# Kernel optimization log

Hardware: AMD Instinct MI355X
Metric: run time of the kernel (lower is better)

The kernel has to match this reference:

```python
import jax, jax.numpy as jnp
import numpy as np

BS, HID, INP, SPAN, OUT, DAYS = 32768, 128, 64, 8, 2, 20


def _init(key, shape, fan_in):
    # mimic torch default uniform(-1/sqrt(fan), 1/sqrt(fan)) init
    bound = 1.0 / np.sqrt(fan_in)
    return jax.random.uniform(key, shape, jnp.float32, -bound, bound)


def setup_inputs() -> dict:
    key = jax.random.key(0)
    ks = jax.random.split(key, 11)
    return {
        "hx": jax.random.normal(ks[0], (BS, HID), jnp.float32),
        # GRUCell params (PyTorch layout: gates stacked [r, z, n])
        "w_ih": _init(ks[1], (3 * HID, INP), HID),
        "w_hh": _init(ks[2], (3 * HID, HID), HID),
        "b_ih": _init(ks[3], (3 * HID,), HID),
        "b_hh": _init(ks[4], (3 * HID,), HID),
        # fc_in: hid -> input
        "fc_in_w": _init(ks[5], (INP, HID), HID),
        "fc_in_b": _init(ks[6], (INP,), HID),
        # fc_out: hid -> out
        "fc_out_w": _init(ks[7], (OUT, HID), HID),
        "fc_out_b": _init(ks[8], (OUT,), HID),
        # num_span_layer: hid -> num_span_classes
        "span_w": _init(ks[9], (SPAN, HID), HID),
        "span_b": _init(ks[10], (SPAN,), HID),
    }


def _gru_cell(x, h, w_ih, w_hh, b_ih, b_hh):
    gi = x @ w_ih.T + b_ih  # [B, 3H]
    gh = h @ w_hh.T + b_hh  # [B, 3H]
    i_r, i_z, i_n = jnp.split(gi, 3, axis=-1)
    h_r, h_z, h_n = jnp.split(gh, 3, axis=-1)
    r = jax.nn.sigmoid(i_r + h_r)
    z = jax.nn.sigmoid(i_z + h_z)
    n = jnp.tanh(i_n + r * h_n)
    return (1.0 - z) * n + z * h


def reference(hx, w_ih, w_hh, b_ih, b_hh, fc_in_w, fc_in_b,
              fc_out_w, fc_out_b, span_w, span_b):
    num_spans = jax.nn.softmax(hx @ span_w.T + span_b, axis=-1)  # [B, SPAN]
    x0 = jnp.zeros((hx.shape[0], fc_in_w.shape[0]), hx.dtype)  # zero first input

    def step(carry, _):
        h, x = carry
        h = _gru_cell(x, h, w_ih, w_hh, b_ih, b_hh)
        x = jax.nn.relu(h @ fc_in_w.T + fc_in_b)
        out = jax.nn.softmax(h @ fc_out_w.T + fc_out_b, axis=-1)  # [B, OUT]
        return (h, x), out

    _, outs = jax.lax.scan(step, (hx, x0), None, length=DAYS)  # [DAYS, B, OUT]
    outputs = jnp.transpose(outs, (1, 0, 2))  # [B, DAYS, OUT]
    return num_spans, outputs
```

## Files before the change

### kernel.cpp

```cpp
#include <hip/hip_runtime.h>
#include <hip/hip_bf16.h>

#define HID 128
#define INP 64
#define SPANN 8
#define NOUT 2
#define DAYS 20
#define RT 4
#define ROWS (16*RT)
#define NTH 512

typedef __attribute__((ext_vector_type(8))) short short8;
typedef __attribute__((ext_vector_type(4))) float f32x4;
typedef __attribute__((ext_vector_type(2))) float f32x2;
typedef unsigned int u32;
typedef __attribute__((ext_vector_type(2))) u32 u32x2;
typedef unsigned short u16;

#define MFMA(a,b,c) __builtin_amdgcn_mfma_f32_16x16x32_bf16(a,b,c,0,0,0)
#define RCPF(x)  __builtin_amdgcn_rcpf(x)
#define EXP2F(x) __builtin_amdgcn_exp2f(x)
#define LOG2E  1.4426950408889634f
#define LOG2E2 2.8853900817779268f

__device__ __forceinline__ u32 pack2(float a, float b){
    __hip_bfloat162 h = __float22bfloat162_rn(float2{a, b});
    u32 r; __builtin_memcpy(&r, &h, 4); return r;
}
__device__ __forceinline__ float sigf(float x){ return RCPF(1.0f + EXP2F(-LOG2E * x)); }
__device__ __forceinline__ float tanhf_(float x){ return fmaf(-2.0f, RCPF(1.0f + EXP2F(LOG2E2 * x)), 1.0f); }

union frag_u { short8 s; u32 w[4]; };
__device__ __forceinline__ short8 ldfrag(const float* p){
    const f32x4 a = *(const f32x4*)p;
    const f32x4 b = *(const f32x4*)(p+4);
    frag_u f;
    f.w[0] = pack2(a[0],a[1]); f.w[1] = pack2(a[2],a[3]);
    f.w[2] = pack2(b[0],b[1]); f.w[3] = pack2(b[2],b[3]);
    return f.s;
}


__global__ __launch_bounds__(NTH, 2) void gru_mfma(
    const float* __restrict__ hx, const float* __restrict__ w_ih,
    const float* __restrict__ w_hh, const float* __restrict__ b_ih,
    const float* __restrict__ b_hh, const float* __restrict__ fc_in_w,
    const float* __restrict__ fc_in_b, const float* __restrict__ fc_out_w,
    const float* __restrict__ fc_out_b, const float* __restrict__ span_w,
    const float* __restrict__ span_b, float* __restrict__ out, int bs)
{
    __shared__ u16 hL[2][RT*2048];
    __shared__ u16 xL[RT*1024];
    __shared__ u16 finL[4*4*64*8];
    __shared__ __attribute__((aligned(16))) float diffP[ROWS][8];

    const int tid = threadIdx.x;
    const int wid = tid >> 6;
    const int l   = tid & 63;
    const int r15 = l & 15;
    const int hi  = l >> 4;
    const int row0 = blockIdx.x * ROWS;
    const int mB  = wid & 3;
    const int rtB_off = wid >> 2;

    short8 whhR[4], whhZ[4], whhN[4];
    short8 wihR[2], wihZ[2], wihN[2];
    const int g0 = wid*16 + r15;
    #pragma unroll
    for (int ks = 0; ks < 4; ++ks){
        whhR[ks] = ldfrag(w_hh + (size_t)(      g0)*HID + ks*32 + hi*8);
        whhZ[ks] = ldfrag(w_hh + (size_t)(128 + g0)*HID + ks*32 + hi*8);
        whhN[ks] = ldfrag(w_hh + (size_t)(256 + g0)*HID + ks*32 + hi*8);
    }
    #pragma unroll
    for (int ks = 0; ks < 2; ++ks){
        wihR[ks] = ldfrag(w_ih + (size_t)(      g0)*INP + ks*32 + hi*8);
        wihZ[ks] = ldfrag(w_ih + (size_t)(128 + g0)*INP + ks*32 + hi*8);
        wihN[ks] = ldfrag(w_ih + (size_t)(256 + g0)*INP + ks*32 + hi*8);
    }

    for (int s = tid; s < 1024; s += NTH) {
        const int mt = s >> 8, ks = (s >> 6) & 3, ll = s & 63;
        short8 f = ldfrag(fc_in_w + (size_t)(mt*16 + (ll&15))*HID + ks*32 + (ll>>4)*8);
        *((short8*)finL + s) = f;
    }

    f32x4 bRv, bZv, bNiv, bNhv, fbv, wd4;
    const int c0 = wid*16 + hi*4;
    #pragma unroll
    for (int q = 0; q < 4; ++q){
        const int g = c0 + q;
        bRv[q]  = b_ih[g]       + b_hh[g];
        bZv[q]  = b_ih[128 + g] + b_hh[128 + g];
        bNiv[q] = b_ih[256 + g];
        bNhv[q] = b_hh[256 + g];
        fbv[q]  = fc_in_b[mB*16 + hi*4 + q];
        wd4[q]  = fc_out_w[g] - fc_out_w[HID + g];
    }
    const float bd = fc_out_b[0] - fc_out_b[1];

    const int wu32  = (wid>>1)*256 + (((wid&1)*2 + (hi>>1))*16 + r15)*4 + (hi&1)*2;
    const int xwu32 = (mB >>1)*256 + (((mB &1)*2 + (hi>>1))*16 + r15)*4 + (hi&1)*2;

    f32x4 hOld0, hOld1, hOld2, hOld3;
    {
        #define LOADH(RTG, HO) do { \
            const f32x4 h4 = *(const f32x4*)(hx + (size_t)(row0 + (RTG)*16 + r15)*HID + c0); \
            HO = h4; \
            u32x2 wv; wv[0] = pack2(h4[0], h4[1]); wv[1] = pack2(h4[2], h4[3]); \
            *(u32x2*)((u32*)&hL[0][(RTG)*2048] + wu32) = wv; } while(0)
        LOADH(0, hOld0); LOADH(1, hOld1); LOADH(2, hOld2); LOADH(3, hOld3);
        #undef LOADH
        u32* xb = (u32*)&xL[0];
        for (int i = tid; i < RT*512; i += NTH) xb[i] = 0u;
    }
    __syncthreads();

    if (wid < 4){
        const short8 zz = {0,0,0,0,0,0,0,0};
        short8 spw[4];
        #pragma unroll
        for (int ks = 0; ks < 4; ++ks)
            spw[ks] = (r15 < SPANN) ? ldfrag(span_w + (size_t)r15*HID + ks*32 + hi*8) : zz;
        f32x4 acc = {0.f,0.f,0.f,0.f};
        #pragma unroll
        for (int q = 0; q < 4; ++q) if (hi < 2) acc[q] = span_b[hi*4 + q];
        const short8* hf = (const short8*)&hL[0][wid*2048];
        #pragma unroll
        for (int ks = 0; ks < 4; ++ks) acc = MFMA(spw[ks], hf[ks*64 + l], acc);
        if (hi < 2){
            float m = fmaxf(fmaxf(acc[0], acc[1]), fmaxf(acc[2], acc[3]));
            m = fmaxf(m, __shfl_xor(m, 16));
            float e0 = EXP2F(LOG2E*(acc[0]-m)), e1 = EXP2F(LOG2E*(acc[1]-m));
            float e2 = EXP2F(LOG2E*(acc[2]-m)), e3 = EXP2F(LOG2E*(acc[3]-m));
            float s = e0 + e1 + e2 + e3;
            s += __shfl_xor(s, 16);
            const float inv = RCPF(s);
            f32x4 o = {e0*inv, e1*inv, e2*inv, e3*inv};
            *(f32x4*)(out + (size_t)(row0 + wid*16 + r15)*SPANN + hi*4) = o;
        }
    }

    float* __restrict__ outp = out + (size_t)bs * SPANN;

    #define TILE_A(RTG, hRd_, hWr_, HO) do { \
        const short8* hf = (const short8*)((hRd_) + (RTG)*2048); \
        const short8* xf = (const short8*)(xL + (RTG)*1024); \
        const short8 h0=hf[l], h1=hf[64+l], h2=hf[128+l], h3=hf[192+l]; \
        const short8 x0=xf[l], x1=xf[64+l]; \
        f32x4 aR  = MFMA(whhR[0], h0, bRv); \
        f32x4 aZ  = MFMA(whhZ[0], h0, bZv); \
        f32x4 aNh = MFMA(whhN[0], h0, bNhv); \
        aR = MFMA(whhR[1],h1,aR); aZ = MFMA(whhZ[1],h1,aZ); aNh = MFMA(whhN[1],h1,aNh); \
        aR = MFMA(whhR[2],h2,aR); aZ = MFMA(whhZ[2],h2,aZ); aNh = MFMA(whhN[2],h2,aNh); \
        aR = MFMA(whhR[3],h3,aR); aZ = MFMA(whhZ[3],h3,aZ); aNh = MFMA(whhN[3],h3,aNh); \
        f32x4 aNi = MFMA(wihN[0], x0, bNiv); \
        aR = MFMA(wihR[0],x0,aR); aZ = MFMA(wihZ[0],x0,aZ); \
        aNi = MFMA(wihN[1],x1,aNi); \
        aR = MFMA(wihR[1],x1,aR); aZ = MFMA(wihZ[1],x1,aZ); \
        float hn[4]; \
        _Pragma("unroll") for (int q=0;q<4;++q){ \
            const float rg = sigf(aR[q]); const float zg = sigf(aZ[q]); \
            const float nn = tanhf_(fmaf(rg, aNh[q], aNi[q])); \
            hn[q] = fmaf(zg, HO[q]-nn, nn); HO[q] = hn[q]; } \
        u32x2 wv; wv[0]=pack2(hn[0],hn[1]); wv[1]=pack2(hn[2],hn[3]); \
        *(u32x2*)((hWr_) + (RTG)*1024 + wu32) = wv; \
        float pd = hn[0]*wd4[0]; pd = fmaf(hn[1],wd4[1],pd); \
        pd = fmaf(hn[2],wd4[2],pd); pd = fmaf(hn[3],wd4[3],pd); \
        pd += __shfl_xor(pd, 16); pd += __shfl_xor(pd, 32); \
        if (hi == 0) diffP[(RTG)*16 + r15][wid] = pd; \
    } while(0)

    #define OUT_STORE(d_, gb_) do { \
        if (wid == 7 && l < 32) { \
            const int rowIdx = (gb_)*32 + l; \
            const f32x4 v0 = *(const f32x4*)&diffP[rowIdx][0]; \
            const f32x4 v1 = *(const f32x4*)&diffP[rowIdx][4]; \
            const float s = ((v0[0]+v0[1])+(v0[2]+v0[3])) + ((v1[0]+v1[1])+(v1[2]+v1[3])); \
            const float p0 = sigf(s + bd); \
            f32x2 o = {p0, 1.0f - p0}; \
            *(f32x2*)(outp + ((size_t)(row0 + rowIdx)*DAYS + (d_))*NOUT) = o; \
        } \
    } while(0)

    #define TILE_B(d_, gb_, hSrc) do { \
        if ((d_) < DAYS-1) { \
            const int rtB = 2*(gb_) + rtB_off; \
            const short8* hf = (const short8*)((hSrc) + rtB*2048); \
            const short8 h0=hf[l], h1=hf[64+l], h2=hf[128+l], h3=hf[192+l]; \
            const short8* fp = (const short8*)finL + mB*256 + l; \
            f32x4 ax = MFMA(fp[0],   h0, fbv); \
            ax       = MFMA(fp[64],  h1, ax); \
            ax       = MFMA(fp[128], h2, ax); \
            ax       = MFMA(fp[192], h3, ax); \
            u32x2 wv; \
            wv[0] = pack2(fmaxf(ax[0],0.f), fmaxf(ax[1],0.f)); \
            wv[1] = pack2(fmaxf(ax[2],0.f), fmaxf(ax[3],0.f)); \
            *(u32x2*)((u32*)xL + rtB*512 + xwu32) = wv; \
        } \
        OUT_STORE(d_, gb_); \
    } while(0)

    #pragma unroll 2
    for (int d = 0; d < DAYS; ++d){
        const u16* hRd = hL[d & 1];
        u32*       hWr = (u32*)hL[(d & 1) ^ 1];

        TILE_A(0, hRd, hWr, hOld0);
        TILE_A(1, hRd, hWr, hOld1);
        if (d > 0) TILE_B(d-1, 1, hRd);
        __syncthreads();

        TILE_A(2, hRd, hWr, hOld2);
        TILE_A(3, hRd, hWr, hOld3);
        TILE_B(d, 0, (const u16*)hWr);
        __syncthreads();
    }
    OUT_STORE(DAYS-1, 1);

    #undef TILE_A
    #undef TILE_B
    #undef OUT_STORE
}

extern "C" void kernel_launch(void* const* d_in, const int* in_sizes, int n_in,
                              void* d_out, int out_size, void* d_ws, size_t ws_size,
                              hipStream_t stream) {
    const float* hx       = (const float*)d_in[0];
    const float* w_ih     = (const float*)d_in[1];
    const float* w_hh     = (const float*)d_in[2];
    const float* b_ih     = (const float*)d_in[3];
    const float* b_hh     = (const float*)d_in[4];
    const float* fc_in_w  = (const float*)d_in[5];
    const float* fc_in_b  = (const float*)d_in[6];
    const float* fc_out_w = (const float*)d_in[7];
    const float* fc_out_b = (const float*)d_in[8];
    const float* span_w   = (const float*)d_in[9];
    const float* span_b   = (const float*)d_in[10];
    float* out = (float*)d_out;

    const int bs = in_sizes[0] / HID;
    dim3 grid(bs / ROWS), block(NTH);
    gru_mfma<<<grid, block, 0, stream>>>(hx, w_ih, w_hh, b_ih, b_hh,
                                         fc_in_w, fc_in_b, fc_out_w, fc_out_b,
                                         span_w, span_b, out, bs);
}
```

Before: 143.9 us.

## Fold exp2 scaling into weights and reload old hidden from LDS

New measurement: 143.3 us (median of 2 runs). Within noise of the previous version (-0.4%).

```diff
diff --git a/kernel.cpp b/kernel.cpp
--- a/kernel.cpp
+++ b/kernel.cpp
@@ -20,23 +20,25 @@
 #define MFMA(a,b,c) __builtin_amdgcn_mfma_f32_16x16x32_bf16(a,b,c,0,0,0)
 #define RCPF(x)  __builtin_amdgcn_rcpf(x)
 #define EXP2F(x) __builtin_amdgcn_exp2f(x)
-#define LOG2E  1.4426950408889634f
-#define LOG2E2 2.8853900817779268f
+#define LOG2E   1.4426950408889634f
+#define NLOG2E  (-1.4426950408889634f)
+#define LOG2E2  2.8853900817779268f
 
 __device__ __forceinline__ u32 pack2(float a, float b){
     __hip_bfloat162 h = __float22bfloat162_rn(float2{a, b});
     u32 r; __builtin_memcpy(&r, &h, 4); return r;
 }
-__device__ __forceinline__ float sigf(float x){ return RCPF(1.0f + EXP2F(-LOG2E * x)); }
-__device__ __forceinline__ float tanhf_(float x){ return fmaf(-2.0f, RCPF(1.0f + EXP2F(LOG2E2 * x)), 1.0f); }
+__device__ __forceinline__ float asF(u32 u){ union{u32 u; float f;} v; v.u = u; return v.f; }
+__device__ __forceinline__ float sig2(float a){ return RCPF(1.0f + EXP2F(a)); }
+__device__ __forceinline__ float tanh2(float a){ return fmaf(-2.0f, RCPF(1.0f + EXP2F(a)), 1.0f); }
 
 union frag_u { short8 s; u32 w[4]; };
-__device__ __forceinline__ short8 ldfrag(const float* p){
+__device__ __forceinline__ short8 ldfrag(const float* p, float sc){
     const f32x4 a = *(const f32x4*)p;
     const f32x4 b = *(const f32x4*)(p+4);
     frag_u f;
-    f.w[0] = pack2(a[0],a[1]); f.w[1] = pack2(a[2],a[3]);
-    f.w[2] = pack2(b[0],b[1]); f.w[3] = pack2(b[2],b[3]);
+    f.w[0] = pack2(sc*a[0],sc*a[1]); f.w[1] = pack2(sc*a[2],sc*a[3]);
+    f.w[2] = pack2(sc*b[0],sc*b[1]); f.w[3] = pack2(sc*b[2],sc*b[3]);
     return f.s;
 }
 
@@ -52,7 +54,7 @@
     __shared__ u16 hL[2][RT*2048];
     __shared__ u16 xL[RT*1024];
     __shared__ u16 finL[4*4*64*8];
-    __shared__ __attribute__((aligned(16))) float diffP[ROWS][8];
+    __shared__ float diffP[ROWS][9];
 
     const int tid = threadIdx.x;
     const int wid = tid >> 6;
@@ -68,20 +70,20 @@
     const int g0 = wid*16 + r15;
     #pragma unroll
     for (int ks = 0; ks < 4; ++ks){
-        whhR[ks] = ldfrag(w_hh + (size_t)(      g0)*HID + ks*32 + hi*8);
-        whhZ[ks] = ldfrag(w_hh + (size_t)(128 + g0)*HID + ks*32 + hi*8);
-        whhN[ks] = ldfrag(w_hh + (size_t)(256 + g0)*HID + ks*32 + hi*8);
+        whhR[ks] = ldfrag(w_hh + (size_t)(      g0)*HID + ks*32 + hi*8, NLOG2E);
+        whhZ[ks] = ldfrag(w_hh + (size_t)(128 + g0)*HID + ks*32 + hi*8, NLOG2E);
+        whhN[ks] = ldfrag(w_hh + (size_t)(256 + g0)*HID + ks*32 + hi*8, LOG2E2);
     }
     #pragma unroll
     for (int ks = 0; ks < 2; ++ks){
-        wihR[ks] = ldfrag(w_ih + (size_t)(      g0)*INP + ks*32 + hi*8);
-        wihZ[ks] = ldfrag(w_ih + (size_t)(128 + g0)*INP + ks*32 + hi*8);
-        wihN[ks] = ldfrag(w_ih + (size_t)(256 + g0)*INP + ks*32 + hi*8);
+        wihR[ks] = ldfrag(w_ih + (size_t)(      g0)*INP + ks*32 + hi*8, NLOG2E);
+        wihZ[ks] = ldfrag(w_ih + (size_t)(128 + g0)*INP + ks*32 + hi*8, NLOG2E);
+        wihN[ks] = ldfrag(w_ih + (size_t)(256 + g0)*INP + ks*32 + hi*8, LOG2E2);
     }
 
     for (int s = tid; s < 1024; s += NTH) {
         const int mt = s >> 8, ks = (s >> 6) & 3, ll = s & 63;
-        short8 f = ldfrag(fc_in_w + (size_t)(mt*16 + (ll&15))*HID + ks*32 + (ll>>4)*8);
+        short8 f = ldfrag(fc_in_w + (size_t)(mt*16 + (ll&15))*HID + ks*32 + (ll>>4)*8, 1.0f);
         *((short8*)finL + s) = f;
     }
 
@@ -90,27 +92,25 @@
     #pragma unroll
     for (int q = 0; q < 4; ++q){
         const int g = c0 + q;
-        bRv[q]  = b_ih[g]       + b_hh[g];
-        bZv[q]  = b_ih[128 + g] + b_hh[128 + g];
-        bNiv[q] = b_ih[256 + g];
-        bNhv[q] = b_hh[256 + g];
+        bRv[q]  = NLOG2E*(b_ih[g]       + b_hh[g]);
+        bZv[q]  = NLOG2E*(b_ih[128 + g] + b_hh[128 + g]);
+        bNiv[q] = LOG2E2* b_ih[256 + g];
+        bNhv[q] = LOG2E2* b_hh[256 + g];
         fbv[q]  = fc_in_b[mB*16 + hi*4 + q];
-        wd4[q]  = fc_out_w[g] - fc_out_w[HID + g];
-    }
-    const float bd = fc_out_b[0] - fc_out_b[1];
+        wd4[q]  = NLOG2E*(fc_out_w[g] - fc_out_w[HID + g]);
+    }
+    const float bd = NLOG2E*(fc_out_b[0] - fc_out_b[1]);
 
     const int wu32  = (wid>>1)*256 + (((wid&1)*2 + (hi>>1))*16 + r15)*4 + (hi&1)*2;
     const int xwu32 = (mB >>1)*256 + (((mB &1)*2 + (hi>>1))*16 + r15)*4 + (hi&1)*2;
 
-    f32x4 hOld0, hOld1, hOld2, hOld3;
     {
-        #define LOADH(RTG, HO) do { \
-            const f32x4 h4 = *(const f32x4*)(hx + (size_t)(row0 + (RTG)*16 + r15)*HID + c0); \
-            HO = h4; \
-            u32x2 wv; wv[0] = pack2(h4[0], h4[1]); wv[1] = pack2(h4[2], h4[3]); \
-            *(u32x2*)((u32*)&hL[0][(RTG)*2048] + wu32) = wv; } while(0)
-        LOADH(0, hOld0); LOADH(1, hOld1); LOADH(2, hOld2); LOADH(3, hOld3);
-        #undef LOADH
+        #pragma unroll
+        for (int rt = 0; rt < RT; ++rt){
+            const f32x4 h4 = *(const f32x4*)(hx + (size_t)(row0 + rt*16 + r15)*HID + c0);
+            u32x2 wv; wv[0] = pack2(h4[0], h4[1]); wv[1] = pack2(h4[2], h4[3]);
+            *(u32x2*)((u32*)&hL[0][rt*2048] + wu32) = wv;
+        }
         u32* xb = (u32*)&xL[0];
         for (int i = tid; i < RT*512; i += NTH) xb[i] = 0u;
     }
@@ -121,7 +121,7 @@
         short8 spw[4];
         #pragma unroll
         for (int ks = 0; ks < 4; ++ks)
-            spw[ks] = (r15 < SPANN) ? ldfrag(span_w + (size_t)r15*HID + ks*32 + hi*8) : zz;
+            spw[ks] = (r15 < SPANN) ? ldfrag(span_w + (size_t)r15*HID + ks*32 + hi*8, 1.0f) : zz;
         f32x4 acc = {0.f,0.f,0.f,0.f};
         #pragma unroll
         for (int q = 0; q < 4; ++q) if (hi < 2) acc[q] = span_b[hi*4 + q];
@@ -143,11 +143,12 @@
 
     float* __restrict__ outp = out + (size_t)bs * SPANN;
 
-    #define TILE_A(RTG, hRd_, hWr_, HO) do { \
+    #define TILE_A(RTG, hRd_, hWr_) do { \
         const short8* hf = (const short8*)((hRd_) + (RTG)*2048); \
         const short8* xf = (const short8*)(xL + (RTG)*1024); \
         const short8 h0=hf[l], h1=hf[64+l], h2=hf[128+l], h3=hf[192+l]; \
         const short8 x0=xf[l], x1=xf[64+l]; \
+        const u32x2 ho = *(const u32x2*)((const u32*)(hRd_) + (RTG)*1024 + wu32); \
         f32x4 aR  = MFMA(whhR[0], h0, bRv); \
         f32x4 aZ  = MFMA(whhZ[0], h0, bZv); \
         f32x4 aNh = MFMA(whhN[0], h0, bNhv); \
@@ -158,11 +159,13 @@
         aR = MFMA(wihR[0],x0,aR); aZ = MFMA(wihZ[0],x0,aZ); \
         aNi = MFMA(wihN[1],x1,aNi); \
         aR = MFMA(wihR[1],x1,aR); aZ = MFMA(wihZ[1],x1,aZ); \
+        const float hold[4] = { asF(ho[0]<<16), asF(ho[0]&0xFFFF0000u), \
+                                asF(ho[1]<<16), asF(ho[1]&0xFFFF0000u) }; \
         float hn[4]; \
         _Pragma("unroll") for (int q=0;q<4;++q){ \
-            const float rg = sigf(aR[q]); const float zg = sigf(aZ[q]); \
-            const float nn = tanhf_(fmaf(rg, aNh[q], aNi[q])); \
-            hn[q] = fmaf(zg, HO[q]-nn, nn); HO[q] = hn[q]; } \
+            const float rg = sig2(aR[q]); const float zg = sig2(aZ[q]); \
+            const float nn = tanh2(fmaf(rg, aNh[q], aNi[q])); \
+            hn[q] = fmaf(zg, hold[q]-nn, nn); } \
         u32x2 wv; wv[0]=pack2(hn[0],hn[1]); wv[1]=pack2(hn[2],hn[3]); \
         *(u32x2*)((hWr_) + (RTG)*1024 + wu32) = wv; \
         float pd = hn[0]*wd4[0]; pd = fmaf(hn[1],wd4[1],pd); \
@@ -174,10 +177,9 @@
     #define OUT_STORE(d_, gb_) do { \
         if (wid == 7 && l < 32) { \
             const int rowIdx = (gb_)*32 + l; \
-            const f32x4 v0 = *(const f32x4*)&diffP[rowIdx][0]; \
-            const f32x4 v1 = *(const f32x4*)&diffP[rowIdx][4]; \
-            const float s = ((v0[0]+v0[1])+(v0[2]+v0[3])) + ((v1[0]+v1[1])+(v1[2]+v1[3])); \
-            const float p0 = sigf(s + bd); \
+            const float* dp = &diffP[rowIdx][0]; \
+            const float s = ((dp[0]+dp[1])+(dp[2]+dp[3])) + ((dp[4]+dp[5])+(dp[6]+dp[7])); \
+            const float p0 = sig2(s + bd); \
             f32x2 o = {p0, 1.0f - p0}; \
             *(f32x2*)(outp + ((size_t)(row0 + rowIdx)*DAYS + (d_))*NOUT) = o; \
         } \
@@ -201,18 +203,18 @@
         OUT_STORE(d_, gb_); \
     } while(0)
 
-    #pragma unroll 2
+    #pragma unroll 1
     for (int d = 0; d < DAYS; ++d){
         const u16* hRd = hL[d & 1];
         u32*       hWr = (u32*)hL[(d & 1) ^ 1];
 
-        TILE_A(0, hRd, hWr, hOld0);
-        TILE_A(1, hRd, hWr, hOld1);
+        TILE_A(0, hRd, hWr);
+        TILE_A(1, hRd, hWr);
         if (d > 0) TILE_B(d-1, 1, hRd);
         __syncthreads();
 
-        TILE_A(2, hRd, hWr, hOld2);
-        TILE_A(3, hRd, hWr, hOld3);
+        TILE_A(2, hRd, hWr);
+        TILE_A(3, hRd, hWr);
         TILE_B(d, 0, (const u16*)hWr);
         __syncthreads();
     }
```
